# Kernel tuning notes

Hardware: AMD Instinct MI355X
Metric: run time of the kernel (lower is better)

## Reference

```python
import jax, jax.numpy as jnp
import numpy as np
import math

B, C, H, W = 4, 128, 180, 180
CCAM, HEADS, DH, N = 256, 4, 32, 20000
HD = HEADS * DH
GAMMA = 0.08
EPS = 1e-6


def setup_inputs() -> dict:
    key = jax.random.key(0)
    ks = jax.random.split(key, 10)
    return {
        "lidar_bev": jax.random.normal(ks[0], (B, C, H, W), jnp.float32),
        "cam_bev_tokens": jax.random.normal(ks[1], (B, N, CCAM), jnp.float32),
        "gate_weights": jax.random.uniform(ks[2], (B, N), jnp.float32),
        "range_alpha": jax.random.uniform(ks[3], (1, 1, H, W), jnp.float32),
        # q_proj: Conv2d(C, HD, 1) -> weight [HD, C] (1x1 conv == per-pixel linear), bias [HD]
        "q_w": jax.random.normal(ks[4], (HD, C), jnp.float32) * 0.02,
        "q_bias": jax.random.normal(ks[5], (HD,), jnp.float32) * 0.02,
        # k/v_proj: Linear(CCAM, HD, bias=False)
        "k_w": jax.random.normal(ks[6], (HD, CCAM), jnp.float32) * 0.02,
        "v_w": jax.random.normal(ks[7], (HD, CCAM), jnp.float32) * 0.02,
        # out: Conv2d(HD, C, 1, bias=False) -> W_out [C, HD]
        "out_w": jax.random.normal(ks[8], (C, HD), jnp.float32) * 0.02,
        "cam_bev_indices": jax.random.randint(ks[9], (B, N, 2), 0, H, jnp.int32),
    }


def reference(lidar_bev, cam_bev_tokens, gate_weights, range_alpha,
              q_w, q_bias, k_w, v_w, out_w, cam_bev_indices):
    scale = 1.0 / math.sqrt(DH)
    # 1x1 conv q projection -> [B, h, d, H*W]
    q = jnp.einsum('bchw,oc->bohw', lidar_bev, q_w) + q_bias[None, :, None, None]
    q = q.reshape(B, HEADS, DH, H * W)

    i = jnp.clip(cam_bev_indices[..., 0], 0, H - 1)
    j = jnp.clip(cam_bev_indices[..., 1], 0, W - 1)
    lin = i * W + j  # [B, N]

    # gather q at sparse BEV locations -> [B, h, d, N]
    q_g = jnp.take_along_axis(q, lin[:, None, None, :], axis=3)

    # k/v projections -> [B, h, d, N]
    k = jnp.einsum('bnc,oc->bno', cam_bev_tokens, k_w).reshape(B, N, HEADS, DH).transpose(0, 2, 3, 1)
    v = jnp.einsum('bnc,oc->bno', cam_bev_tokens, v_w).reshape(B, N, HEADS, DH).transpose(0, 2, 3, 1)

    # elementwise-multiply attention: logits [B, h, N], softmax over the N tokens
    attn = jax.nn.softmax((q_g * k).sum(axis=2) * scale, axis=-1) * gate_weights[:, None, :]
    fused = (attn[:, :, None, :] * v).reshape(B, HD, N)  # [B, h*d, N]
    out_tok = jnp.einsum('co,bon->bcn', out_w, fused)    # [B, C, N]

    # per-batch scatter (index_add) + hit counts (bincount)
    def scatter_b(tok, lin_b):
        df = jnp.zeros((C, H * W), tok.dtype).at[:, lin_b].add(tok)
        hits = jnp.zeros((H * W,), tok.dtype).at[lin_b].add(1.0)
        return df, hits

    delta_flat, hits = jax.vmap(scatter_b)(out_tok, lin)  # [B,C,HW], [B,HW]
    mask = (hits > 0).astype(lidar_bev.dtype)  # [B, HW]

    # mean over hit locations (per batch, per channel), subtract on hits only
    mean_on = (delta_flat * mask[:, None, :]).sum(axis=-1, keepdims=True) \
              / (mask.sum(axis=-1)[:, None, None] + EPS)  # [B, C, 1]
    tmp = (delta_flat - mean_on * mask[:, None, :]).reshape(B, C, H, W)
    tmp = tmp * range_alpha * GAMMA
    return lidar_bev + tmp
```

## Files before the change

kernel.cpp:

```cpp
#include <hip/hip_runtime.h>

#define BB 4
#define CC 128
#define HH 180
#define WWW 180
#define HWHW (HH*WWW)
#define CCAMD 256
#define NHEADS 4
#define HDD 128
#define NT 20000
#define MTOT 80000
#define GAMMA_C 0.08f
#define EPS_C 1e-6f
#define SCALE_C 0.17677669529663687f

typedef short bf16x8 __attribute__((ext_vector_type(8)));
typedef float f32x4 __attribute__((ext_vector_type(4)));

typedef __attribute__((address_space(1))) const unsigned int GU;
typedef __attribute__((address_space(3))) unsigned int LU;

static __device__ __forceinline__ void gll16(const void* g, void* l) {
  __builtin_amdgcn_global_load_lds((GU*)g, (LU*)l, 16, 0, 0);
}

#define WAIT_VMCNT0() asm volatile("s_waitcnt vmcnt(0)" ::: "memory")
#define WAIT_VMCNT2() asm volatile("s_waitcnt vmcnt(2)" ::: "memory")
#define WAIT_VMCNT3() asm volatile("s_waitcnt vmcnt(3)" ::: "memory")
#define WAIT_LGKM0()  asm volatile("s_waitcnt lgkmcnt(0)" ::: "memory")

static __device__ __forceinline__ unsigned short f2bf(float x) {
  unsigned int b = __float_as_uint(x);
  unsigned int r = (b + 0x7fffu + ((b >> 16) & 1u)) >> 16;
  return (unsigned short)r;
}
static __device__ __forceinline__ float b2f(unsigned short u) {
  return __uint_as_float(((unsigned int)u) << 16);
}

static __device__ __forceinline__ float warpMax(float v) {
#pragma unroll
  for (int o = 32; o >= 1; o >>= 1) v = fmaxf(v, __shfl_xor(v, o));
  return v;
}
static __device__ __forceinline__ float warpSum(float v) {
#pragma unroll
  for (int o = 32; o >= 1; o >>= 1) v += __shfl_xor(v, o);
  return v;
}
static __device__ __forceinline__ int warpSumI(int v) {
#pragma unroll
  for (int o = 32; o >= 1; o >>= 1) v += __shfl_xor(v, o);
  return v;
}

__global__ __launch_bounds__(256) void k_prep_pix(
    const float* __restrict__ kw, const float* __restrict__ vw,
    const float* __restrict__ qw, const float* __restrict__ ow,
    unsigned short* __restrict__ kvw, unsigned short* __restrict__ qwb,
    unsigned short* __restrict__ owb, const int* __restrict__ cidx,
    int* __restrict__ pix_ws, int* __restrict__ cnt_pix)
{
  if (blockIdx.x < 96) {
    const int t = blockIdx.x * 256 + threadIdx.x;
    float4 f;
    unsigned short* dst;
    if (t < 16384) {
      f = (t < 8192) ? ((const float4*)kw)[t] : ((const float4*)vw)[t - 8192];
      dst = kvw + (size_t)t * 4;
    } else if (t < 20480) {
      const int i = t - 16384;
      f = ((const float4*)qw)[i];
      dst = qwb + (size_t)i * 4;
    } else {
      const int i = t - 20480;
      f = ((const float4*)ow)[i];
      dst = owb + (size_t)i * 4;
    }
    ushort4 u;
    u.x = f2bf(f.x); u.y = f2bf(f.y); u.z = f2bf(f.z); u.w = f2bf(f.w);
    *(ushort4*)dst = u;
  } else {
    const int t = (blockIdx.x - 96) * 256 + threadIdx.x;
    if (t >= MTOT) return;
    const int2 ij = *(const int2*)(cidx + (size_t)t * 2);
    int ii = ij.x; ii = ii < 0 ? 0 : (ii > HH - 1 ? HH - 1 : ii);
    int jj = ij.y; jj = jj < 0 ? 0 : (jj > WWW - 1 ? WWW - 1 : jj);
    const int pix = ii * WWW + jj;
    pix_ws[t] = pix;
    atomicAdd(cnt_pix + (size_t)(t / NT) * HWHW + pix, 1);
  }
}

__global__ __launch_bounds__(512) void k_tr2b(
    const float* __restrict__ lidar, unsigned short* __restrict__ lidar_t)
{
  const int idx = blockIdx.x * 512 + threadIdx.x;
  if (idx >= BB * HWHW) return;
  const int b = idx / HWHW, p = idx - b * HWHW;
  const float* src = lidar + (size_t)b * CC * HWHW + p;
  unsigned short* dst = lidar_t + (size_t)idx * 128;
#pragma unroll
  for (int c8 = 0; c8 < 16; ++c8) {
    bf16x8 v;
#pragma unroll
    for (int e = 0; e < 8; ++e)
      v[e] = (short)f2bf(src[(size_t)(c8 * 8 + e) * HWHW]);
    ((bf16x8*)dst)[c8] = v;
  }
}

__global__ __launch_bounds__(512) void k_scanA(
    const int* __restrict__ cnt, int* __restrict__ bsum,
    float* __restrict__ cntB)
{
  const int b = blockIdx.y, blk = blockIdx.x;
  const int idx = blk * 512 + threadIdx.x;
  int v = (idx < HWHW) ? cnt[(size_t)b * HWHW + idx] : 0;
  int h = (v > 0) ? 1 : 0;
  v = warpSumI(v);
  h = warpSumI(h);
  __shared__ int ws[8], hs[8];
  const int wave = threadIdx.x >> 6, lane = threadIdx.x & 63;
  if (lane == 0) { ws[wave] = v; hs[wave] = h; }
  __syncthreads();
  if (threadIdx.x == 0) {
    int sv = 0, sh = 0;
#pragma unroll
    for (int w = 0; w < 8; ++w) { sv += ws[w]; sh += hs[w]; }
    bsum[b * 64 + blk] = sv;
    atomicAdd(cntB + b, (float)sh);
  }
}

__global__ __launch_bounds__(64) void k_scanB(
    const int* __restrict__ bsum, int* __restrict__ boff)
{
  const int b = blockIdx.x, t = threadIdx.x;
  const int v = bsum[b * 64 + t];
  int inc = v;
#pragma unroll
  for (int off = 1; off < 64; off <<= 1) {
    int u = __shfl_up(inc, off, 64);
    if (t >= off) inc += u;
  }
  boff[b * 64 + t] = inc - v;
}

template<int KSTEPS, int KW, int AMODE, int EPI, int NOUT>
static __device__ void pipe_body(
    int mblk, int nblk, unsigned short* lds,
    const float* __restrict__ Af32, const unsigned short* __restrict__ Abf,
    const unsigned short* __restrict__ Bw, const float* __restrict__ bias,
    unsigned short* __restrict__ Dbf, const int* __restrict__ pixw,
    float* __restrict__ aux, const unsigned short* __restrict__ kvb,
    float* __restrict__ meanr, const float* __restrict__ smMp,
    const float* __restrict__ smSinvp, const float* __restrict__ gatep,
    const float* __restrict__ logp, const int* __restrict__ sortn)
{
  const int tid = threadIdx.x;
  const int lane = tid & 63, wave = tid >> 6;
  const int wm = wave >> 2, wn = wave & 3;
  const int l16 = lane & 15, kg = lane >> 4;
  const int sr_rd = (l16 >> 1) & 3;

  const int row_s = wave * 16 + (lane >> 2);
  const int chunk_s = lane & 3;
  const int swz_s = chunk_s ^ ((lane >> 3) & 3);
  const int a_dst = row_s * 32 + swz_s * 8;

  const unsigned short* bsrc = Bw + (size_t)(nblk * 128 + row_s) * KW + swz_s * 8;

  const float* asrc_f32 = nullptr;
  const unsigned short* asrc_bf = nullptr;
  float coef4[4] = {0.f, 0.f, 0.f, 0.f};
  if constexpr (AMODE == 0) {
    asrc_f32 = Af32 + (size_t)(mblk * 128 + row_s) * KW + chunk_s * 8;
  } else if constexpr (AMODE == 2) {
    const int r = mblk * 128 + row_s;
    const int bb = r / NT;
    asrc_bf = Abf + ((size_t)bb * HWHW + pixw[r]) * 128 + swz_s * 8;
  } else {
    const int r = mblk * 128 + row_s;
    const int bb = r / NT, pos = r - bb * NT;
    const int n = sortn[(size_t)bb * NT + pos];
    asrc_bf = Abf + ((size_t)bb * NT + n) * 256 + 128 + chunk_s * 8;
    const float ga = gatep[(size_t)bb * NT + n];
#pragma unroll
    for (int h = 0; h < 4; ++h) {
      const int bh = bb * NHEADS + h;
      coef4[h] = __expf(logp[(size_t)bh * NT + n] - smMp[bh]) * smSinvp[bh] * ga;
    }
  }

  f32x4 acc[4][2];
#pragma unroll
  for (int i = 0; i < 4; ++i)
#pragma unroll
    for (int j = 0; j < 2; ++j) acc[i][j] = (f32x4)0.0f;

  float4 afx[2], afy[2];
  bf16x8 av[2];

  auto issueA = [&](int kt, int s, int buf) {
    if constexpr (AMODE == 0) {
      afx[s] = *(const float4*)(asrc_f32 + kt * 32);
      afy[s] = *(const float4*)(asrc_f32 + kt * 32 + 4);
    } else if constexpr (AMODE == 2) {
      gll16(asrc_bf + kt * 32, &lds[buf * 8192 + wave * 512]);
    } else {
      av[s] = *(const bf16x8*)(asrc_bf + kt * 32);
    }
  };
  auto issueB = [&](int kt, int buf) {
    gll16(bsrc + kt * 32, &lds[buf * 8192 + 4096 + wave * 512]);
  };
  auto writeA = [&](int kt, int s, int buf) {
    bf16x8 v;
    if constexpr (AMODE == 0) {
      v[0] = (short)f2bf(afx[s].x); v[1] = (short)f2bf(afx[s].y);
      v[2] = (short)f2bf(afx[s].z); v[3] = (short)f2bf(afx[s].w);
      v[4] = (short)f2bf(afy[s].x); v[5] = (short)f2bf(afy[s].y);
      v[6] = (short)f2bf(afy[s].z); v[7] = (short)f2bf(afy[s].w);
    } else {
      const float c = coef4[kt];
#pragma unroll
      for (int e = 0; e < 8; ++e)
        v[e] = (short)f2bf(b2f((unsigned short)av[s][e]) * c);
    }
    *(bf16x8*)&lds[buf * 8192 + a_dst] = v;
  };
  auto compute = [&](int buf) {
    const int base = buf * 8192;
    bf16x8 a[4], b[2];
#pragma unroll
    for (int mf = 0; mf < 4; ++mf) {
      const int row = wm * 64 + mf * 16 + l16;
      a[mf] = *(const bf16x8*)&lds[base + row * 32 + ((kg ^ sr_rd) << 3)];
    }
#pragma unroll
    for (int nf = 0; nf < 2; ++nf) {
      const int row = wn * 32 + nf * 16 + l16;
      b[nf] = *(const bf16x8*)&lds[base + 4096 + row * 32 + ((kg ^ sr_rd) << 3)];
    }
#pragma unroll
    for (int mf = 0; mf < 4; ++mf)
#pragma unroll
      for (int nf = 0; nf < 2; ++nf)
        acc[mf][nf] =
            __builtin_amdgcn_mfma_f32_16x16x32_bf16(a[mf], b[nf], acc[mf][nf], 0, 0, 0);
  };

  issueA(0, 0, 0); issueB(0, 0);
  issueA(1, 1, 1); issueB(1, 1);
  if constexpr (AMODE != 2) writeA(0, 0, 0);

#pragma unroll
  for (int t = 0; t < KSTEPS; ++t) {
    if (t < KSTEPS - 1) {
      if constexpr (AMODE == 0) WAIT_VMCNT3(); else WAIT_VMCNT2();
    } else {
      WAIT_VMCNT0();
    }
    WAIT_LGKM0();
    __builtin_amdgcn_s_barrier();
    __builtin_amdgcn_sched_barrier(0);
    if (t + 2 < KSTEPS) {
      issueA(t + 2, t & 1, (t + 2) % 3);
      issueB(t + 2, (t + 2) % 3);
    }
    compute(t % 3);
    if constexpr (AMODE != 2) {
      if (t + 1 < KSTEPS) writeA(t + 1, (t + 1) & 1, (t + 1) % 3);
    }
  }
  __syncthreads();

  float* scratch = (float*)lds;

  if constexpr (EPI == 0) {
#pragma unroll
    for (int mf = 0; mf < 4; ++mf) {
#pragma unroll
      for (int j = 0; j < 4; ++j) {
        const int row = mblk * 128 + wm * 64 + mf * 16 + kg * 4 + j;
        unsigned short* dr = Dbf + (size_t)row * NOUT + nblk * 128 + wn * 32 + l16;
#pragma unroll
        for (int nf = 0; nf < 2; ++nf)
          dr[nf * 16] = f2bf(acc[mf][nf][j]);
      }
    }
  } else if constexpr (EPI == 2) {
    float bv[2];
#pragma unroll
    for (int nf = 0; nf < 2; ++nf)
      bv[nf] = bias[wn * 32 + nf * 16 + l16];
#pragma unroll
    for (int mf = 0; mf < 4; ++mf) {
#pragma unroll
      for (int j = 0; j < 4; ++j) {
        const int rl = wm * 64 + mf * 16 + kg * 4 + j;
        const int row = mblk * 128 + rl;
        const unsigned short* kr = kvb + (size_t)row * 256 + wn * 32 + l16;
        float s = (acc[mf][0][j] + bv[0]) * b2f(kr[0]) +
                  (acc[mf][1][j] + bv[1]) * b2f(kr[16]);
        s += __shfl_xor(s, 8, 16); s += __shfl_xor(s, 4, 16);
        s += __shfl_xor(s, 2, 16); s += __shfl_xor(s, 1, 16);
        if (l16 == 0) scratch[rl * 4 + wn] = s;
      }
    }
    __syncthreads();
    if (tid < 128) {
      const int row = mblk * 128 + tid;
      const int bb = row / NT, n = row - bb * NT;
#pragma unroll
      for (int h = 0; h < 4; ++h)
        aux[((size_t)bb * NHEADS + h) * NT + n] = scratch[tid * 4 + h] * SCALE_C;
    }
  } else {
    if (tid < 256) scratch[tid] = 0.0f;
    __syncthreads();
    const int b0 = (mblk * 128) / NT;
#pragma unroll
    for (int mf = 0; mf < 4; ++mf) {
      const int baser = mblk * 128 + wm * 64 + mf * 16 + kg * 4;
      const int bb = baser / NT;
      const int bsel = (bb != b0) ? 1 : 0;
      float s[2] = {0.0f, 0.0f};
#pragma unroll
      for (int j = 0; j < 4; ++j) {
        const int row = baser + j;
        unsigned short* dr = Dbf + (size_t)row * 128 + wn * 32 + l16;
#pragma unroll
        for (int nf = 0; nf < 2; ++nf) {
          dr[nf * 16] = f2bf(acc[mf][nf][j]);
          s[nf] += acc[mf][nf][j];
        }
      }
#pragma unroll
      for (int nf = 0; nf < 2; ++nf)
        atomicAdd(&scratch[bsel * 128 + wn * 32 + nf * 16 + l16], s[nf]);
    }
    __syncthreads();
    const int b1 = (mblk * 128 + 127) / NT;
    if (tid < 128) atomicAdd(meanr + (size_t)b0 * 128 + tid, scratch[tid]);
    else if (tid < 256 && b1 != b0)
      atomicAdd(meanr + (size_t)b1 * 128 + (tid - 128), scratch[tid]);
  }
}

__global__ __launch_bounds__(512) void k_kv(
    const float* __restrict__ tokens, const unsigned short* __restrict__ kvw,
    unsigned short* __restrict__ kv_bf)
{
  __shared__ unsigned short lds[24576];
  pipe_body<8, 256, 0, 0, 256>(blockIdx.x, blockIdx.y, lds, tokens, nullptr,
                               kvw, nullptr, kv_bf, nullptr, nullptr,
                               nullptr, nullptr, nullptr, nullptr,
                               nullptr, nullptr, nullptr);
}

__global__ __launch_bounds__(512) void k_m2(
    const int* __restrict__ cnt_pix, const int* __restrict__ boff,
    int* __restrict__ start, const unsigned short* __restrict__ lidar_t,
    const unsigned short* __restrict__ qwb, const float* __restrict__ qb,
    const int* __restrict__ pixw, float* __restrict__ logits,
    const unsigned short* __restrict__ kv_bf)
{
  __shared__ unsigned short lds[24576];
  const int bid = blockIdx.x;
  if (bid < 256) {
    __shared__ int ws[8];
    const int b = bid >> 6, blk = bid & 63;
    const int idx = blk * 512 + threadIdx.x;
    const int wave = threadIdx.x >> 6, lane = threadIdx.x & 63;
    int v = (idx < HWHW) ? cnt_pix[(size_t)b * HWHW + idx] : 0;
    int inc = v;
#pragma unroll
    for (int off = 1; off < 64; off <<= 1) {
      int u = __shfl_up(inc, off, 64);
      if (lane >= off) inc += u;
    }
    if (lane == 63) ws[wave] = inc;
    __syncthreads();
    int wo = 0;
#pragma unroll
    for (int w = 0; w < 8; ++w)
      if (w < wave) wo += ws[w];
    if (idx < HWHW)
      start[(size_t)b * HWHW + idx] = boff[b * 64 + blk] + wo + inc - v;
  } else {
    pipe_body<4, 128, 2, 2, 128>(bid - 256, 0, lds, nullptr, lidar_t, qwb,
                                 qb, nullptr, pixw, logits, kv_bf, nullptr,
                                 nullptr, nullptr, nullptr, nullptr, nullptr);
  }
}

__global__ __launch_bounds__(256) void k_m3(
    const float* __restrict__ logits, float* __restrict__ pm,
    float* __restrict__ ps, const int* __restrict__ pix_ws,
    const int* __restrict__ start, int* __restrict__ fill,
    int* __restrict__ sortn)
{
  const int bid = blockIdx.x;
  if (bid < 128) {
    const int ch = bid & 7, bh = bid >> 3;
    const float* L = logits + (size_t)bh * NT + ch * 2500;
    const int tid = threadIdx.x;
    __shared__ float sred[4];

    float m = -INFINITY;
    for (int i = tid; i < 2500; i += 256) m = fmaxf(m, L[i]);
    m = warpMax(m);
    if ((tid & 63) == 0) sred[tid >> 6] = m;
    __syncthreads();
    m = fmaxf(fmaxf(sred[0], sred[1]), fmaxf(sred[2], sred[3]));

    float s = 0.0f;
    for (int i = tid; i < 2500; i += 256) s += __expf(L[i] - m);
    s = warpSum(s);
    __syncthreads();
    if ((tid & 63) == 0) sred[tid >> 6] = s;
    __syncthreads();
    if (tid == 0) {
      pm[bh * 8 + ch] = m;
      ps[bh * 8 + ch] = sred[0] + sred[1] + sred[2] + sred[3];
    }
  } else {
    const int t = (bid - 128) * 256 + threadIdx.x;
    if (t >= MTOT) return;
    const int b = t / NT, n = t - b * NT;
    const int pix = pix_ws[t];
    const int pos = atomicAdd(fill + (size_t)b * HWHW + pix, 1);
    sortn[(size_t)b * NT + start[(size_t)b * HWHW + pix] + pos] = n;
  }
}

__global__ __launch_bounds__(64) void k_smfix(
    const float* __restrict__ pm, const float* __restrict__ ps,
    float* __restrict__ smM, float* __restrict__ smSinv)
{
  const int t = threadIdx.x;
  if (t >= BB * NHEADS) return;
  float M = -INFINITY;
#pragma unroll
  for (int c = 0; c < 8; ++c) M = fmaxf(M, pm[t * 8 + c]);
  float S = 0.0f;
#pragma unroll
  for (int c = 0; c < 8; ++c) S += ps[t * 8 + c] * __expf(pm[t * 8 + c] - M);
  smM[t] = M;
  smSinv[t] = 1.0f / S;
}

__global__ __launch_bounds__(512) void k_out(
    const unsigned short* __restrict__ kv_bf, const unsigned short* __restrict__ owb,
    unsigned short* __restrict__ out_tok, float* __restrict__ meanr,
    const float* __restrict__ smM, const float* __restrict__ smSinv,
    const float* __restrict__ gate, const float* __restrict__ logits,
    const int* __restrict__ sortn)
{
  __shared__ unsigned short lds[24576];
  pipe_body<4, 128, 4, 3, 128>(blockIdx.x, 0, lds, nullptr, kv_bf, owb,
                               nullptr, out_tok, nullptr, nullptr, nullptr,
                               meanr, smM, smSinv, gate, logits, sortn);
}

__global__ __launch_bounds__(512) void k_final2(
    const float* __restrict__ lidar, const float* __restrict__ alpha,
    const int* __restrict__ cnt_pix, const int* __restrict__ start,
    const unsigned short* __restrict__ out_tok,
    const float* __restrict__ mean_raw, const float* __restrict__ cntB,
    float* __restrict__ out)
{
  __shared__ float tile[80 * 136];
  const int b = blockIdx.y;
  const int p0 = blockIdx.x * 80;
  const int t = threadIdx.x;

  const int g = t >> 5, l32 = t & 31;
#pragma unroll
  for (int i = 0; i < 5; ++i) {
    const int pl = i * 16 + g;
    const int p = p0 + pl;
    const int st = start[(size_t)b * HWHW + p];
    const int cn = cnt_pix[(size_t)b * HWHW + p];
    float4 a = make_float4(0.0f, 0.0f, 0.0f, 0.0f);
    const unsigned short* rp = out_tok + ((size_t)b * NT + st) * 128 + l32 * 4;
    for (int k = 0; k < cn; ++k) {
      const ushort4 u = *(const ushort4*)(rp + (size_t)k * 128);
      a.x += b2f(u.x); a.y += b2f(u.y); a.z += b2f(u.z); a.w += b2f(u.w);
    }
    *(float4*)&tile[pl * 136 + ((l32 ^ (pl & 7)) << 2)] = a;
  }
  __syncthreads();

  const int c = t >> 2, sub = t & 3;
  const int cq = c >> 2, cr = c & 3;
  const float mn = mean_raw[b * 128 + c] / (cntB[b] + EPS_C);
  const size_t cbase = ((size_t)b * CC + c) * HWHW + p0;
  const int* cnb = cnt_pix + (size_t)b * HWHW + p0;
#pragma unroll
  for (int j = 0; j < 5; ++j) {
    const int pq = j * 16 + sub * 4;
    float4 d;
    d.x = tile[(pq + 0) * 136 + (((cq ^ ((pq + 0) & 7)) << 2) | cr)];
    d.y = tile[(pq + 1) * 136 + (((cq ^ ((pq + 1) & 7)) << 2) | cr)];
    d.z = tile[(pq + 2) * 136 + (((cq ^ ((pq + 2) & 7)) << 2) | cr)];
    d.w = tile[(pq + 3) * 136 + (((cq ^ ((pq + 3) & 7)) << 2) | cr)];
    const float4 li = *(const float4*)(lidar + cbase + pq);
    const float4 al = *(const float4*)(alpha + p0 + pq);
    const int4 hc = *(const int4*)(cnb + pq);
    float4 o;
    o.x = li.x + (d.x - (hc.x > 0 ? mn : 0.0f)) * al.x * GAMMA_C;
    o.y = li.y + (d.y - (hc.y > 0 ? mn : 0.0f)) * al.y * GAMMA_C;
    o.z = li.z + (d.z - (hc.z > 0 ? mn : 0.0f)) * al.z * GAMMA_C;
    o.w = li.w + (d.w - (hc.w > 0 ? mn : 0.0f)) * al.w * GAMMA_C;
    *(float4*)(out + cbase + pq) = o;
  }
}

extern "C" void kernel_launch(void* const* d_in, const int* in_sizes, int n_in,
                              void* d_out, int out_size, void* d_ws, size_t ws_size,
                              hipStream_t stream)
{
  const float* lidar  = (const float*)d_in[0];
  const float* tokens = (const float*)d_in[1];
  const float* gate   = (const float*)d_in[2];
  const float* alpha  = (const float*)d_in[3];
  const float* q_w    = (const float*)d_in[4];
  const float* q_b    = (const float*)d_in[5];
  const float* k_w    = (const float*)d_in[6];
  const float* v_w    = (const float*)d_in[7];
  const float* out_w  = (const float*)d_in[8];
  const int*   cidx   = (const int*)d_in[9];
  float* out = (float*)d_out;

  char* W = (char*)d_ws;
  unsigned short* kv_bf   = (unsigned short*)(W + 0);
  unsigned short* lidar_t = (unsigned short*)(W + 40960000);
  unsigned short* out_tok = (unsigned short*)(W + 74137600);
  float* logits  = (float*)(W + 94617600);
  int*   pix_ws  = (int*)(W + 95897600);
  int*   sortn   = (int*)(W + 96217600);
  int*   cnt_pix = (int*)(W + 96537600);
  int*   start   = (int*)(W + 97056000);
  int*   fill    = (int*)(W + 97574400);
  float* mean_raw = (float*)(W + 98092800);
  float* cntB     = (float*)(W + 98094848);
  unsigned short* kvw_bf = (unsigned short*)(W + 98094912);
  unsigned short* qw_bf  = (unsigned short*)(W + 98225984);
  unsigned short* ow_bf  = (unsigned short*)(W + 98258752);
  float* pm     = (float*)(W + 98291520);
  float* ps     = (float*)(W + 98292032);
  float* smM    = (float*)(W + 98292544);
  float* smSinv = (float*)(W + 98292608);
  int*   bsum   = (int*)(W + 98292672);
  int*   boff   = (int*)(W + 98293696);

  hipMemsetAsync(cnt_pix, 0, (size_t)BB * HWHW * sizeof(int), stream);
  hipMemsetAsync(fill, 0, (size_t)BB * HWHW * sizeof(int), stream);
  hipMemsetAsync(mean_raw, 0, 2048 + 64, stream);

  k_prep_pix<<<dim3(409), 256, 0, stream>>>(k_w, v_w, q_w, out_w, kvw_bf,
                                            qw_bf, ow_bf, cidx, pix_ws, cnt_pix);
  k_tr2b<<<dim3(254), 512, 0, stream>>>(lidar, lidar_t);
  k_scanA<<<dim3(64, BB), 512, 0, stream>>>(cnt_pix, bsum, cntB);
  k_scanB<<<dim3(BB), 64, 0, stream>>>(bsum, boff);
  k_kv<<<dim3(625, 2), 512, 0, stream>>>(tokens, kvw_bf, kv_bf);
  k_m2<<<dim3(881), 512, 0, stream>>>(cnt_pix, boff, start, lidar_t, qw_bf,
                                      q_b, pix_ws, logits, kv_bf);
  k_m3<<<dim3(441), 256, 0, stream>>>(logits, pm, ps, pix_ws, start, fill, sortn);
  k_smfix<<<dim3(1), 64, 0, stream>>>(pm, ps, smM, smSinv);
  k_out<<<dim3(625), 512, 0, stream>>>(kv_bf, ow_bf, out_tok, mean_raw,
                                       smM, smSinv, gate, logits, sortn);
  k_final2<<<dim3(405, BB), 512, 0, stream>>>(lidar, alpha, cnt_pix, start,
                                              out_tok, mean_raw, cntB, out);
}
```

Measured before the change: 184.7 us.

## Fuse K/V projection into Q-logit kernel, keep K tile in LDS

```diff
diff --git a/kernel.cpp b/kernel.cpp
--- a/kernel.cpp
+++ b/kernel.cpp
@@ -149,14 +149,14 @@
 
 template<int KSTEPS, int KW, int AMODE, int EPI, int NOUT>
 static __device__ void pipe_body(
-    int mblk, int nblk, unsigned short* lds,
+    int mblk, int nblk, unsigned short* lds, unsigned short* kld,
     const float* __restrict__ Af32, const unsigned short* __restrict__ Abf,
     const unsigned short* __restrict__ Bw, const float* __restrict__ bias,
     unsigned short* __restrict__ Dbf, const int* __restrict__ pixw,
-    float* __restrict__ aux, const unsigned short* __restrict__ kvb,
-    float* __restrict__ meanr, const float* __restrict__ smMp,
-    const float* __restrict__ smSinvp, const float* __restrict__ gatep,
-    const float* __restrict__ logp, const int* __restrict__ sortn)
+    float* __restrict__ aux, float* __restrict__ meanr,
+    const float* __restrict__ smMp, const float* __restrict__ smSinvp,
+    const float* __restrict__ gatep, const float* __restrict__ logp,
+    const int* __restrict__ sortn)
 {
   const int tid = threadIdx.x;
   const int lane = tid & 63, wave = tid >> 6;
@@ -184,7 +184,7 @@
     const int r = mblk * 128 + row_s;
     const int bb = r / NT, pos = r - bb * NT;
     const int n = sortn[(size_t)bb * NT + pos];
-    asrc_bf = Abf + ((size_t)bb * NT + n) * 256 + 128 + chunk_s * 8;
+    asrc_bf = Abf + ((size_t)bb * NT + n) * KW + chunk_s * 8;
     const float ga = gatep[(size_t)bb * NT + n];
 #pragma unroll
     for (int h = 0; h < 4; ++h) {
@@ -290,34 +290,7 @@
           dr[nf * 16] = f2bf(acc[mf][nf][j]);
       }
     }
-  } else if constexpr (EPI == 2) {
-    float bv[2];
-#pragma unroll
-    for (int nf = 0; nf < 2; ++nf)
-      bv[nf] = bias[wn * 32 + nf * 16 + l16];
-#pragma unroll
-    for (int mf = 0; mf < 4; ++mf) {
-#pragma unroll
-      for (int j = 0; j < 4; ++j) {
-        const int rl = wm * 64 + mf * 16 + kg * 4 + j;
-        const int row = mblk * 128 + rl;
-        const unsigned short* kr = kvb + (size_t)row * 256 + wn * 32 + l16;
-        float s = (acc[mf][0][j] + bv[0]) * b2f(kr[0]) +
-                  (acc[mf][1][j] + bv[1]) * b2f(kr[16]);
-        s += __shfl_xor(s, 8, 16); s += __shfl_xor(s, 4, 16);
-        s += __shfl_xor(s, 2, 16); s += __shfl_xor(s, 1, 16);
-        if (l16 == 0) scratch[rl * 4 + wn] = s;
-      }
-    }
-    __syncthreads();
-    if (tid < 128) {
-      const int row = mblk * 128 + tid;
-      const int bb = row / NT, n = row - bb * NT;
-#pragma unroll
-      for (int h = 0; h < 4; ++h)
-        aux[((size_t)bb * NHEADS + h) * NT + n] = scratch[tid * 4 + h] * SCALE_C;
-    }
-  } else {
+  } else if constexpr (EPI == 3) {
     if (tid < 256) scratch[tid] = 0.0f;
     __syncthreads();
     const int b0 = (mblk * 128) / NT;
@@ -346,28 +319,56 @@
     if (tid < 128) atomicAdd(meanr + (size_t)b0 * 128 + tid, scratch[tid]);
     else if (tid < 256 && b1 != b0)
       atomicAdd(meanr + (size_t)b1 * 128 + (tid - 128), scratch[tid]);
-  }
-}
-
-__global__ __launch_bounds__(512) void k_kv(
+  } else if constexpr (EPI == 4) {
+#pragma unroll
+    for (int mf = 0; mf < 4; ++mf) {
+#pragma unroll
+      for (int j = 0; j < 4; ++j) {
+        const int rl = wm * 64 + mf * 16 + kg * 4 + j;
+#pragma unroll
+        for (int nf = 0; nf < 2; ++nf)
+          kld[rl * 128 + wn * 32 + nf * 16 + l16] = f2bf(acc[mf][nf][j]);
+      }
+    }
+  } else {
+    float bv[2];
+#pragma unroll
+    for (int nf = 0; nf < 2; ++nf)
+      bv[nf] = bias[wn * 32 + nf * 16 + l16];
+#pragma unroll
+    for (int mf = 0; mf < 4; ++mf) {
+#pragma unroll
+      for (int j = 0; j < 4; ++j) {
+        const int rl = wm * 64 + mf * 16 + kg * 4 + j;
+        float s = (acc[mf][0][j] + bv[0]) * b2f(kld[rl * 128 + wn * 32 + l16]) +
+                  (acc[mf][1][j] + bv[1]) * b2f(kld[rl * 128 + wn * 32 + 16 + l16]);
+        s += __shfl_xor(s, 8, 16); s += __shfl_xor(s, 4, 16);
+        s += __shfl_xor(s, 2, 16); s += __shfl_xor(s, 1, 16);
+        if (l16 == 0) scratch[rl * 4 + wn] = s;
+      }
+    }
+    __syncthreads();
+    if (tid < 128) {
+      const int row = mblk * 128 + tid;
+      const int bb = row / NT, n = row - bb * NT;
+#pragma unroll
+      for (int h = 0; h < 4; ++h)
+        aux[((size_t)bb * NHEADS + h) * NT + n] = scratch[tid * 4 + h] * SCALE_C;
+    }
+  }
+}
+
+__global__ __launch_bounds__(512) void k_fkvq(
+    const int* __restrict__ cnt_pix, const int* __restrict__ boff,
+    int* __restrict__ start,
     const float* __restrict__ tokens, const unsigned short* __restrict__ kvw,
-    unsigned short* __restrict__ kv_bf)
+    unsigned short* __restrict__ v_bf,
+    const unsigned short* __restrict__ lidar_t,
+    const unsigned short* __restrict__ qwb, const float* __restrict__ qb,
+    const int* __restrict__ pixw, float* __restrict__ logits)
 {
   __shared__ unsigned short lds[24576];
-  pipe_body<8, 256, 0, 0, 256>(blockIdx.x, blockIdx.y, lds, tokens, nullptr,
-                               kvw, nullptr, kv_bf, nullptr, nullptr,
-                               nullptr, nullptr, nullptr, nullptr,
-                               nullptr, nullptr, nullptr);
-}
-
-__global__ __launch_bounds__(512) void k_m2(
-    const int* __restrict__ cnt_pix, const int* __restrict__ boff,
-    int* __restrict__ start, const unsigned short* __restrict__ lidar_t,
-    const unsigned short* __restrict__ qwb, const float* __restrict__ qb,
-    const int* __restrict__ pixw, float* __restrict__ logits,
-    const unsigned short* __restrict__ kv_bf)
-{
-  __shared__ unsigned short lds[24576];
+  __shared__ unsigned short kld[16384];
   const int bid = blockIdx.x;
   if (bid < 256) {
     __shared__ int ws[8];
@@ -390,8 +391,16 @@
     if (idx < HWHW)
       start[(size_t)b * HWHW + idx] = boff[b * 64 + blk] + wo + inc - v;
   } else {
-    pipe_body<4, 128, 2, 2, 128>(bid - 256, 0, lds, nullptr, lidar_t, qwb,
-                                 qb, nullptr, pixw, logits, kv_bf, nullptr,
+    const int mblk = bid - 256;
+    pipe_body<8, 256, 0, 4, 128>(mblk, 0, lds, kld, tokens, nullptr, kvw,
+                                 nullptr, nullptr, nullptr, nullptr, nullptr,
+                                 nullptr, nullptr, nullptr, nullptr, nullptr);
+    pipe_body<8, 256, 0, 0, 128>(mblk, 0, lds, nullptr, tokens, nullptr,
+                                 kvw + (size_t)128 * CCAMD, nullptr, v_bf,
+                                 nullptr, nullptr, nullptr, nullptr, nullptr,
+                                 nullptr, nullptr, nullptr);
+    pipe_body<4, 128, 2, 5, 128>(mblk, 0, lds, kld, nullptr, lidar_t, qwb,
+                                 qb, nullptr, pixw, logits, nullptr,
                                  nullptr, nullptr, nullptr, nullptr, nullptr);
   }
 }
@@ -453,15 +462,15 @@
 }
 
 __global__ __launch_bounds__(512) void k_out(
-    const unsigned short* __restrict__ kv_bf, const unsigned short* __restrict__ owb,
+    const unsigned short* __restrict__ v_bf, const unsigned short* __restrict__ owb,
     unsigned short* __restrict__ out_tok, float* __restrict__ meanr,
     const float* __restrict__ smM, const float* __restrict__ smSinv,
     const float* __restrict__ gate, const float* __restrict__ logits,
     const int* __restrict__ sortn)
 {
   __shared__ unsigned short lds[24576];
-  pipe_body<4, 128, 4, 3, 128>(blockIdx.x, 0, lds, nullptr, kv_bf, owb,
-                               nullptr, out_tok, nullptr, nullptr, nullptr,
+  pipe_body<4, 128, 4, 3, 128>(blockIdx.x, 0, lds, nullptr, nullptr, v_bf,
+                               owb, nullptr, out_tok, nullptr, nullptr,
                                meanr, smM, smSinv, gate, logits, sortn);
 }
 
@@ -536,7 +545,7 @@
   float* out = (float*)d_out;
 
   char* W = (char*)d_ws;
-  unsigned short* kv_bf   = (unsigned short*)(W + 0);
+  unsigned short* v_bf    = (unsigned short*)(W + 0);
   unsigned short* lidar_t = (unsigned short*)(W + 40960000);
   unsigned short* out_tok = (unsigned short*)(W + 74137600);
   float* logits  = (float*)(W + 94617600);
@@ -566,12 +575,12 @@
   k_tr2b<<<dim3(254), 512, 0, stream>>>(lidar, lidar_t);
   k_scanA<<<dim3(64, BB), 512, 0, stream>>>(cnt_pix, bsum, cntB);
   k_scanB<<<dim3(BB), 64, 0, stream>>>(bsum, boff);
-  k_kv<<<dim3(625, 2), 512, 0, stream>>>(tokens, kvw_bf, kv_bf);
-  k_m2<<<dim3(881), 512, 0, stream>>>(cnt_pix, boff, start, lidar_t, qw_bf,
-                                      q_b, pix_ws, logits, kv_bf);
+  k_fkvq<<<dim3(881), 512, 0, stream>>>(cnt_pix, boff, start, tokens, kvw_bf,
+                                        v_bf, lidar_t, qw_bf, q_b, pix_ws,
+                                        logits);
   k_m3<<<dim3(441), 256, 0, stream>>>(logits, pm, ps, pix_ws, start, fill, sortn);
   k_smfix<<<dim3(1), 64, 0, stream>>>(pm, ps, smM, smSinv);
-  k_out<<<dim3(625), 512, 0, stream>>>(kv_bf, ow_bf, out_tok, mean_raw,
+  k_out<<<dim3(625), 512, 0, stream>>>(v_bf, ow_bf, out_tok, mean_raw,
                                        smM, smSinv, gate, logits, sortn);
   k_final2<<<dim3(405, BB), 512, 0, stream>>>(lidar, alpha, cnt_pix, start,
                                               out_tok, mean_raw, cntB, out);
```

Measured after the change: 188.3 us. Within noise of the previous version (+1.9%).

## Replace pipelined K/V projection with whole-weight-in-LDS direct-register GEMM kernel

Applied to the files above, without the earlier changes.

```diff
diff --git a/kernel.cpp b/kernel.cpp
--- a/kernel.cpp
+++ b/kernel.cpp
@@ -147,6 +147,89 @@
   boff[b * 64 + t] = inc - v;
 }
 
+__global__ __launch_bounds__(512) void k_kv2(
+    const float* __restrict__ tokens, const unsigned short* __restrict__ kvw,
+    unsigned short* __restrict__ kv_bf)
+{
+  __shared__ unsigned short Bl[128 * 256];
+  const int tid = threadIdx.x;
+  const int lane = tid & 63, wave = tid >> 6;
+  const int wm = wave >> 1, wn = wave & 1;
+  const int l16 = lane & 15, kg = lane >> 4;
+  const int mblk = blockIdx.x, nblk = blockIdx.y;
+
+#pragma unroll
+  for (int i = 0; i < 8; ++i) {
+    const int s = i * 512 + tid;
+    const int row = s >> 5, sc = s & 31;
+    const unsigned short* src =
+        kvw + (size_t)(nblk * 128 + row) * CCAMD + ((sc ^ (row & 7)) << 3);
+    gll16(src, &Bl[(size_t)(i * 512 + wave * 64) * 8]);
+  }
+  WAIT_VMCNT0();
+  __syncthreads();
+
+  const float* a0 =
+      tokens + (size_t)(mblk * 128 + wm * 32 + l16) * CCAMD + kg * 8;
+  const float* a1 = a0 + (size_t)16 * CCAMD;
+
+  f32x4 acc[2][4];
+#pragma unroll
+  for (int i = 0; i < 2; ++i)
+#pragma unroll
+    for (int j = 0; j < 4; ++j) acc[i][j] = (f32x4)0.0f;
+
+#pragma unroll
+  for (int kt = 0; kt < 8; ++kt) {
+    bf16x8 a[2];
+    {
+      const float4 f0 = *(const float4*)(a0 + kt * 32);
+      const float4 f1 = *(const float4*)(a0 + kt * 32 + 4);
+      bf16x8 v;
+      v[0] = (short)f2bf(f0.x); v[1] = (short)f2bf(f0.y);
+      v[2] = (short)f2bf(f0.z); v[3] = (short)f2bf(f0.w);
+      v[4] = (short)f2bf(f1.x); v[5] = (short)f2bf(f1.y);
+      v[6] = (short)f2bf(f1.z); v[7] = (short)f2bf(f1.w);
+      a[0] = v;
+    }
+    {
+      const float4 f0 = *(const float4*)(a1 + kt * 32);
+      const float4 f1 = *(const float4*)(a1 + kt * 32 + 4);
+      bf16x8 v;
+      v[0] = (short)f2bf(f0.x); v[1] = (short)f2bf(f0.y);
+      v[2] = (short)f2bf(f0.z); v[3] = (short)f2bf(f0.w);
+      v[4] = (short)f2bf(f1.x); v[5] = (short)f2bf(f1.y);
+      v[6] = (short)f2bf(f1.z); v[7] = (short)f2bf(f1.w);
+      a[1] = v;
+    }
+    bf16x8 b[4];
+#pragma unroll
+    for (int nf = 0; nf < 4; ++nf) {
+      const int row = wn * 64 + nf * 16 + l16;
+      const int ch = (kt * 4 + kg) ^ (row & 7);
+      b[nf] = *(const bf16x8*)&Bl[row * 256 + ch * 8];
+    }
+#pragma unroll
+    for (int mf = 0; mf < 2; ++mf)
+#pragma unroll
+      for (int nf = 0; nf < 4; ++nf)
+        acc[mf][nf] =
+            __builtin_amdgcn_mfma_f32_16x16x32_bf16(a[mf], b[nf], acc[mf][nf], 0, 0, 0);
+  }
+
+#pragma unroll
+  for (int mf = 0; mf < 2; ++mf) {
+#pragma unroll
+    for (int j = 0; j < 4; ++j) {
+      const int row = mblk * 128 + wm * 32 + mf * 16 + kg * 4 + j;
+      unsigned short* dr = kv_bf + (size_t)row * 256 + nblk * 128 + wn * 64 + l16;
+#pragma unroll
+      for (int nf = 0; nf < 4; ++nf)
+        dr[nf * 16] = f2bf(acc[mf][nf][j]);
+    }
+  }
+}
+
 template<int KSTEPS, int KW, int AMODE, int EPI, int NOUT>
 static __device__ void pipe_body(
     int mblk, int nblk, unsigned short* lds,
@@ -347,17 +430,6 @@
     else if (tid < 256 && b1 != b0)
       atomicAdd(meanr + (size_t)b1 * 128 + (tid - 128), scratch[tid]);
   }
-}
-
-__global__ __launch_bounds__(512) void k_kv(
-    const float* __restrict__ tokens, const unsigned short* __restrict__ kvw,
-    unsigned short* __restrict__ kv_bf)
-{
-  __shared__ unsigned short lds[24576];
-  pipe_body<8, 256, 0, 0, 256>(blockIdx.x, blockIdx.y, lds, tokens, nullptr,
-                               kvw, nullptr, kv_bf, nullptr, nullptr,
-                               nullptr, nullptr, nullptr, nullptr,
-                               nullptr, nullptr, nullptr);
 }
 
 __global__ __launch_bounds__(512) void k_m2(
@@ -566,7 +638,7 @@
   k_tr2b<<<dim3(254), 512, 0, stream>>>(lidar, lidar_t);
   k_scanA<<<dim3(64, BB), 512, 0, stream>>>(cnt_pix, bsum, cntB);
   k_scanB<<<dim3(BB), 64, 0, stream>>>(bsum, boff);
-  k_kv<<<dim3(625, 2), 512, 0, stream>>>(tokens, kvw_bf, kv_bf);
+  k_kv2<<<dim3(625, 2), 512, 0, stream>>>(tokens, kvw_bf, kv_bf);
   k_m2<<<dim3(881), 512, 0, stream>>>(cnt_pix, boff, start, lidar_t, qw_bf,
                                       q_b, pix_ws, logits, kv_bf);
   k_m3<<<dim3(441), 256, 0, stream>>>(logits, pm, ps, pix_ws, start, fill, sortn);
```

Measured after the change: 202.7 us. 1.1x slower.
